# Kernel tuning notes

Measured on AMD Instinct MI355X. Metric: run time of the kernel, lower is better.

The kernel has to match this reference:

```python
import jax, jax.numpy as jnp
import numpy as np

E, B, D = 32, 8192, 256

def setup_inputs() -> dict:
    key = jax.random.key(0)
    k_x, k_c, k_s = jax.random.split(key, 3)
    x = jax.random.normal(k_x, (B, D), dtype=jnp.float32)
    # RandomUniform(-0.5, 0.5) init for both weights
    Centroids = jax.random.uniform(k_c, (E, 1, D), dtype=jnp.float32, minval=-0.5, maxval=0.5)
    A = jax.random.normal(k_s, (E, D, D), dtype=jnp.float32) * 0.1
    # well-conditioned (invertible) covariance-like matrices
    Sigmas = jnp.einsum('eij,ekj->eik', A, A) / D + jnp.eye(D, dtype=jnp.float32)[None]
    return {"x": x, "Centroids": Centroids, "Sigmas": Sigmas}

def reference(x, Centroids, Sigmas):
    # dif: [E, B, D] = broadcasted (x - centroid_e)
    dif = x[None, :, :] - Centroids            # Centroids [E,1,D] broadcasts over B
    inv = jnp.linalg.inv(Sigmas)               # [E, D, D]
    # diagonal of dif @ inv @ dif^T computed directly: [E, B]
    mah = jnp.einsum('ebd,edk,ebk->eb', dif, inv, dif)
    return mah.T                                # [B, E]; activation is None (linear)
```

## Files before the change

kernel.cpp:

```cpp
#include <hip/hip_runtime.h>
#include <stdint.h>


#define NE 32
#define NB 8192
#define DD 256

typedef __bf16 bf16_t;
typedef bf16_t bf16x8 __attribute__((ext_vector_type(8)));
typedef bf16_t bf16x4 __attribute__((ext_vector_type(4)));
typedef float  f32x4  __attribute__((ext_vector_type(4)));
typedef float  f32x16 __attribute__((ext_vector_type(16)));

#define LDX 264
#define LDT 264

static __device__ __forceinline__ void gl2lds16(const void* g, void* l) {
  __builtin_amdgcn_global_load_lds((__attribute__((address_space(1))) void*)(g),
                                   (__attribute__((address_space(3))) void*)(l),
                                   16, 0, 0);
}

__global__ __launch_bounds__(256) void k_x(const float* __restrict__ x,
                                           bf16_t* __restrict__ Xbf) {
  int i8 = (blockIdx.x * 256 + threadIdx.x) * 8;
  f32x4 a = *(const f32x4*)(x + i8);
  f32x4 b = *(const f32x4*)(x + i8 + 4);
  bf16x8 o;
  o[0] = (bf16_t)a[0]; o[1] = (bf16_t)a[1]; o[2] = (bf16_t)a[2]; o[3] = (bf16_t)a[3];
  o[4] = (bf16_t)b[0]; o[5] = (bf16_t)b[1]; o[6] = (bf16_t)b[2]; o[7] = (bf16_t)b[3];
  *(bf16x8*)(Xbf + i8) = o;
}

__global__ __launch_bounds__(512, 2) void k_inv(const float* __restrict__ Sg,
                                                bf16_t* __restrict__ Invbf) {
  int ct = blockIdx.x;
  int e  = blockIdx.y;
  int tid = threadIdx.x, w = tid >> 6, l = tid & 63;
  __shared__ bf16_t Ml[256 * LDX];
  __shared__ bf16_t T2t[32 * LDT];
  const float* Se = Sg + (size_t)e * 65536;

#pragma unroll
  for (int i = 0; i < 16; ++i) {
    int s = i * 512 + tid;
    int row = s >> 5, c8 = (s & 31) * 8;
    f32x4 a = *(const f32x4*)(Se + row * 256 + c8);
    f32x4 b = *(const f32x4*)(Se + row * 256 + c8 + 4);
    float v[8] = {a[0], a[1], a[2], a[3], b[0], b[1], b[2], b[3]};
    int dj = row - c8;
    if (dj >= 0 && dj < 8) v[dj] -= 1.0f;
    bf16x8 o;
#pragma unroll
    for (int j = 0; j < 8; ++j) o[j] = (bf16_t)v[j];
    *(bf16x8*)&Ml[row * LDX + c8] = o;
  }
  __syncthreads();

  int rA = w * 32 + (l & 15);
  int q8 = (l >> 4) * 8;
  int cg0 = ct * 32;

  f32x4 acc1[2][2];
#pragma unroll
  for (int i = 0; i < 2; ++i)
#pragma unroll
    for (int j = 0; j < 2; ++j) acc1[i][j] = (f32x4){0.f, 0.f, 0.f, 0.f};
#pragma unroll
  for (int kk = 0; kk < 256; kk += 32) {
    bf16x8 a0 = *(const bf16x8*)&Ml[rA * LDX + kk + q8];
    bf16x8 a1 = *(const bf16x8*)&Ml[(rA + 16) * LDX + kk + q8];
    bf16x8 b0 = *(const bf16x8*)&Ml[(cg0 + (l & 15)) * LDX + kk + q8];
    bf16x8 b1 = *(const bf16x8*)&Ml[(cg0 + 16 + (l & 15)) * LDX + kk + q8];
    acc1[0][0] = __builtin_amdgcn_mfma_f32_16x16x32_bf16(a0, b0, acc1[0][0], 0, 0, 0);
    acc1[0][1] = __builtin_amdgcn_mfma_f32_16x16x32_bf16(a0, b1, acc1[0][1], 0, 0, 0);
    acc1[1][0] = __builtin_amdgcn_mfma_f32_16x16x32_bf16(a1, b0, acc1[1][0], 0, 0, 0);
    acc1[1][1] = __builtin_amdgcn_mfma_f32_16x16x32_bf16(a1, b1, acc1[1][1], 0, 0, 0);
  }
#pragma unroll
  for (int nf = 0; nf < 2; ++nf) {
    int n0 = w * 32 + nf * 16 + (l >> 4) * 4;
#pragma unroll
    for (int cf = 0; cf < 2; ++cf) {
      int cl = cf * 16 + (l & 15), cg = cg0 + cl;
      bf16x4 mr = *(const bf16x4*)&Ml[cg * LDX + n0];
      f32x4 vv = acc1[nf][cf];
      bf16x4 o;
#pragma unroll
      for (int q = 0; q < 4; ++q) {
        float t2 = (((n0 + q) == cg) ? 1.0f : 0.0f) - (float)mr[q] + vv[q];
        o[q] = (bf16_t)t2;
      }
      *(bf16x4*)&T2t[cl * LDT + n0] = o;
    }
  }
  __syncthreads();

  f32x4 acc2[2][2];
#pragma unroll
  for (int i = 0; i < 2; ++i)
#pragma unroll
    for (int j = 0; j < 2; ++j) acc2[i][j] = (f32x4){0.f, 0.f, 0.f, 0.f};
#pragma unroll
  for (int kk = 0; kk < 256; kk += 32) {
    bf16x8 a0 = *(const bf16x8*)&Ml[rA * LDX + kk + q8];
    bf16x8 a1 = *(const bf16x8*)&Ml[(rA + 16) * LDX + kk + q8];
    bf16x8 b0 = *(const bf16x8*)&T2t[(l & 15) * LDT + kk + q8];
    bf16x8 b1 = *(const bf16x8*)&T2t[(16 + (l & 15)) * LDT + kk + q8];
    acc2[0][0] = __builtin_amdgcn_mfma_f32_16x16x32_bf16(a0, b0, acc2[0][0], 0, 0, 0);
    acc2[0][1] = __builtin_amdgcn_mfma_f32_16x16x32_bf16(a0, b1, acc2[0][1], 0, 0, 0);
    acc2[1][0] = __builtin_amdgcn_mfma_f32_16x16x32_bf16(a1, b0, acc2[1][0], 0, 0, 0);
    acc2[1][1] = __builtin_amdgcn_mfma_f32_16x16x32_bf16(a1, b1, acc2[1][1], 0, 0, 0);
  }
  bf16_t* Ce = Invbf + (size_t)e * 65536;
#pragma unroll
  for (int nf = 0; nf < 2; ++nf) {
    int n0 = w * 32 + nf * 16 + (l >> 4) * 4;
#pragma unroll
    for (int cf = 0; cf < 2; ++cf) {
      int cg = cg0 + cf * 16 + (l & 15);
#pragma unroll
      for (int q = 0; q < 4; ++q) {
        float vv = (((n0 + q) == cg) ? 1.0f : 0.0f) - acc2[nf][cf][q];
        Ce[(cg >> 3) * 2048 + (n0 + q) * 8 + (cg & 7)] = (bf16_t)vv;
      }
    }
  }
}

__global__ __launch_bounds__(256) void k_v(const bf16_t* __restrict__ Invbf,
                                           const float* __restrict__ Cent,
                                           float* __restrict__ v2,
                                           float* __restrict__ s_out) {
  int e = blockIdx.x, d = threadIdx.x;
  __shared__ float cl[256];
  __shared__ float ps[256];
  cl[d] = Cent[e * 256 + d];
  __syncthreads();
  const bf16_t* Ie = Invbf + (size_t)e * 65536 + d * 8;
  float acc = 0.f;
#pragma unroll
  for (int ksl = 0; ksl < 32; ++ksl) {
    bf16x8 r = *(const bf16x8*)(Ie + ksl * 2048);
#pragma unroll
    for (int j = 0; j < 8; ++j) acc += (float)r[j] * cl[ksl * 8 + j];
  }
  v2[e * 256 + d] = 2.0f * acc;
  ps[d] = cl[d] * acc;
  __syncthreads();
  for (int off = 128; off > 0; off >>= 1) {
    if (d < off) ps[d] += ps[d + off];
    __syncthreads();
  }
  if (d == 0) s_out[e] = ps[0];
}

__global__ __launch_bounds__(512, 2) void k_main(const bf16_t* __restrict__ Xbf,
                                                 const bf16_t* __restrict__ Invbf,
                                                 const float* __restrict__ v2g,
                                                 const float* __restrict__ sg,
                                                 float* __restrict__ out) {
  int bt = blockIdx.x;
  int eg = blockIdx.y;
  int tid = threadIdx.x, w = tid >> 6, l = tid & 63;
  __shared__ bf16_t Xl[65536];
  __shared__ bf16_t Invl[2][8192];

  const bf16_t* Xg = Xbf + (size_t)bt * 65536;
  char* Xb = (char*)Xl;

#pragma unroll
  for (int p = 0; p < 16; p += 4) {
    f32x4 t0[4];
#pragma unroll
    for (int i = 0; i < 4; ++i) {
      int s = (p + i) * 512 + tid;
      int row = s >> 5, c16 = s & 31;
      t0[i] = *(const f32x4*)(Xg + row * 256 + c16 * 8);
    }
#pragma unroll
    for (int i = 0; i < 4; ++i) {
      int s = (p + i) * 512 + tid;
      int row = s >> 5, c16 = s & 31;
      int byte = (row * 512 + c16 * 16) ^ ((row & 7) << 4);
      *(f32x4*)(Xb + byte) = t0[i];
    }
  }

  {
    const bf16_t* src = Invbf + (size_t)(eg * 4) * 65536;
    bf16_t* dst = (bf16_t*)Invl[0];
    gl2lds16(src + w * 512 + l * 8,        dst + w * 512);
    gl2lds16(src + 4096 + w * 512 + l * 8, dst + 4096 + w * 512);
  }
  __syncthreads();

  int wn = w >> 2, wb = w & 3;
  int lrow = l & 31, lhalf = l >> 5;
  int nbase = wn * 128;
  int bbase = wb * 64;

  f32x16 acc[4][2];
#pragma unroll
  for (int nf = 0; nf < 4; ++nf)
#pragma unroll
    for (int cf = 0; cf < 2; ++cf)
#pragma unroll
      for (int q = 0; q < 16; ++q) acc[nf][cf][q] = 0.f;

  for (int t = 0; t < 32; ++t) {
    int kk = (t & 7) * 32;
    int cur = t & 1;
    if (t < 31) {
      int tn = t + 1;
      const bf16_t* src = Invbf + (size_t)(eg * 4 + (tn >> 3)) * 65536 + (tn & 7) * 8192;
      bf16_t* dst = (bf16_t*)Invl[tn & 1];
      gl2lds16(src + w * 512 + l * 8,        dst + w * 512);
      gl2lds16(src + 4096 + w * 512 + l * 8, dst + 4096 + w * 512);
    }
    const bf16_t* Ib = (const bf16_t*)Invl[cur];
    bf16x8 af[2][4], bfr[2][2];
#pragma unroll
    for (int s = 0; s < 2; ++s) {
#pragma unroll
      for (int nf = 0; nf < 4; ++nf)
        af[s][nf] = *(const bf16x8*)(Ib + (s * 2 + lhalf) * 2048 + (nbase + nf * 32 + lrow) * 8);
#pragma unroll
      for (int cf = 0; cf < 2; ++cf) {
        int b = bbase + cf * 32 + lrow;
        int byte = (b * 512 + (kk + s * 16 + lhalf * 8) * 2) ^ ((b & 7) << 4);
        bfr[s][cf] = *(const bf16x8*)(Xb + byte);
      }
    }
#pragma unroll
    for (int s = 0; s < 2; ++s)
#pragma unroll
      for (int nf = 0; nf < 4; ++nf)
#pragma unroll
        for (int cf = 0; cf < 2; ++cf)
          acc[nf][cf] = __builtin_amdgcn_mfma_f32_32x32x16_bf16(af[s][nf], bfr[s][cf], acc[nf][cf], 0, 0, 0);

    if ((t & 7) == 7) {
      int e = eg * 4 + (t >> 3);
      float bsum[2] = {0.f, 0.f};
#pragma unroll
      for (int nf = 0; nf < 4; ++nf)
#pragma unroll
        for (int g = 0; g < 4; ++g) {
          int n0 = nbase + nf * 32 + 8 * g + 4 * lhalf;
          f32x4 vv = *(const f32x4*)(v2g + e * 256 + n0);
#pragma unroll
          for (int cf = 0; cf < 2; ++cf) {
            int b = bbase + cf * 32 + lrow;
            int byte = (b * 512 + n0 * 2) ^ ((b & 7) << 4);
            bf16x4 xr = *(const bf16x4*)(Xb + byte);
#pragma unroll
            for (int q = 0; q < 4; ++q)
              bsum[cf] += (float)xr[q] * (acc[nf][cf][g * 4 + q] - vv[q]);
          }
        }
      __syncthreads();
      float* red = (float*)Invl[cur];
#pragma unroll
      for (int cf = 0; cf < 2; ++cf) {
        float r = bsum[cf];
        r += __shfl_xor(r, 32);
        if (lhalf == 0) red[wn * 256 + bbase + cf * 32 + lrow] = r;
      }
      __syncthreads();
      if (tid < 256) {
        float res = sg[e] + red[tid] + red[256 + tid];
        out[(size_t)(bt * 256 + tid) * 32 + e] = res;
      }
#pragma unroll
      for (int nf = 0; nf < 4; ++nf)
#pragma unroll
        for (int cf = 0; cf < 2; ++cf)
#pragma unroll
          for (int q = 0; q < 16; ++q) acc[nf][cf][q] = 0.f;
    }
    __syncthreads();
  }
}

extern "C" void kernel_launch(void* const* d_in, const int* in_sizes, int n_in,
                              void* d_out, int out_size, void* d_ws, size_t ws_size,
                              hipStream_t stream) {
  const float* x    = (const float*)d_in[0];
  const float* cent = (const float*)d_in[1];
  const float* sig  = (const float*)d_in[2];
  float* out = (float*)d_out;

  char* ws = (char*)d_ws;
  bf16_t* Xbf   = (bf16_t*)(ws);
  bf16_t* Invbf = (bf16_t*)(ws + (4ull << 20));
  float*  v2    = (float*)(ws + (8ull << 20));
  float*  sArr  = (float*)(ws + (8ull << 20) + 32768);

  k_x   <<<dim3(1024),   dim3(256), 0, stream>>>(x, Xbf);
  k_inv <<<dim3(8, NE),  dim3(512), 0, stream>>>(sig, Invbf);
  k_v   <<<dim3(NE),     dim3(256), 0, stream>>>(Invbf, cent, v2, sArr);
  k_main<<<dim3(32, 8),  dim3(512), 0, stream>>>(Xbf, Invbf, v2, sArr, out);
}
```

Measured before the change: 72.37 us.

## Fold bf16 conversion of x into inversion kernel and shrink main tiles

Removes the separate x-to-bf16 kernel and does that conversion at the start of each inversion block, saving one launch. The main kernel now uses 128-row batch tiles with 256 threads, giving a 512-block grid instead of 256 blocks so more CUs stay busy. X is staged into LDS with direct global-to-LDS loads using a wider XOR swizzle, and the inverse is streamed in smaller 16-wide K chunks. In exchange there are more pipeline iterations and barriers per block, and each inverse tile is reloaded by twice as many blocks.

Measured after the change: 77.84 us. 1.08x slower.

```diff
diff --git a/kernel.cpp b/kernel.cpp
--- a/kernel.cpp
+++ b/kernel.cpp
@@ -21,18 +21,9 @@
                                    16, 0, 0);
 }
 
-__global__ __launch_bounds__(256) void k_x(const float* __restrict__ x,
-                                           bf16_t* __restrict__ Xbf) {
-  int i8 = (blockIdx.x * 256 + threadIdx.x) * 8;
-  f32x4 a = *(const f32x4*)(x + i8);
-  f32x4 b = *(const f32x4*)(x + i8 + 4);
-  bf16x8 o;
-  o[0] = (bf16_t)a[0]; o[1] = (bf16_t)a[1]; o[2] = (bf16_t)a[2]; o[3] = (bf16_t)a[3];
-  o[4] = (bf16_t)b[0]; o[5] = (bf16_t)b[1]; o[6] = (bf16_t)b[2]; o[7] = (bf16_t)b[3];
-  *(bf16x8*)(Xbf + i8) = o;
-}
-
 __global__ __launch_bounds__(512, 2) void k_inv(const float* __restrict__ Sg,
+                                                const float* __restrict__ x,
+                                                bf16_t* __restrict__ Xbf,
                                                 bf16_t* __restrict__ Invbf) {
   int ct = blockIdx.x;
   int e  = blockIdx.y;
@@ -40,6 +31,22 @@
   __shared__ bf16_t Ml[256 * LDX];
   __shared__ bf16_t T2t[32 * LDT];
   const float* Se = Sg + (size_t)e * 65536;
+
+  {
+    int off = (blockIdx.x + 8 * blockIdx.y) * 8192 + tid * 16;
+    f32x4 a0 = *(const f32x4*)(x + off);
+    f32x4 a1 = *(const f32x4*)(x + off + 4);
+    f32x4 a2 = *(const f32x4*)(x + off + 8);
+    f32x4 a3 = *(const f32x4*)(x + off + 12);
+    bf16x8 o0, o1;
+#pragma unroll
+    for (int j = 0; j < 4; ++j) {
+      o0[j] = (bf16_t)a0[j]; o0[4 + j] = (bf16_t)a1[j];
+      o1[j] = (bf16_t)a2[j]; o1[4 + j] = (bf16_t)a3[j];
+    }
+    *(bf16x8*)(Xbf + off) = o0;
+    *(bf16x8*)(Xbf + off + 8) = o1;
+  }
 
 #pragma unroll
   for (int i = 0; i < 16; ++i) {
@@ -155,47 +162,37 @@
   if (d == 0) s_out[e] = ps[0];
 }
 
-__global__ __launch_bounds__(512, 2) void k_main(const bf16_t* __restrict__ Xbf,
+__global__ __launch_bounds__(256, 2) void k_main(const bf16_t* __restrict__ Xbf,
                                                  const bf16_t* __restrict__ Invbf,
                                                  const float* __restrict__ v2g,
                                                  const float* __restrict__ sg,
                                                  float* __restrict__ out) {
-  int bt = blockIdx.x;
-  int eg = blockIdx.y;
+  int eg = blockIdx.x;
+  int bt = blockIdx.y;
   int tid = threadIdx.x, w = tid >> 6, l = tid & 63;
-  __shared__ bf16_t Xl[65536];
-  __shared__ bf16_t Invl[2][8192];
-
-  const bf16_t* Xg = Xbf + (size_t)bt * 65536;
+  __shared__ bf16_t Xl[128 * 256];
+  __shared__ bf16_t Invl[2][4096];
+
+  const bf16_t* Xg = Xbf + (size_t)bt * 128 * 256;
   char* Xb = (char*)Xl;
 
 #pragma unroll
-  for (int p = 0; p < 16; p += 4) {
-    f32x4 t0[4];
-#pragma unroll
-    for (int i = 0; i < 4; ++i) {
-      int s = (p + i) * 512 + tid;
-      int row = s >> 5, c16 = s & 31;
-      t0[i] = *(const f32x4*)(Xg + row * 256 + c16 * 8);
-    }
-#pragma unroll
-    for (int i = 0; i < 4; ++i) {
-      int s = (p + i) * 512 + tid;
-      int row = s >> 5, c16 = s & 31;
-      int byte = (row * 512 + c16 * 16) ^ ((row & 7) << 4);
-      *(f32x4*)(Xb + byte) = t0[i];
-    }
-  }
-
+  for (int j = 0; j < 16; ++j) {
+    int base = (w * 16 + j) * 1024;
+    int row = (base >> 9) + (l >> 5);
+    int inner = (l & 31) * 16;
+    const char* src = (const char*)Xg + row * 512 + (inner ^ ((row & 31) << 4));
+    gl2lds16(src, Xb + base);
+  }
   {
     const bf16_t* src = Invbf + (size_t)(eg * 4) * 65536;
     bf16_t* dst = (bf16_t*)Invl[0];
-    gl2lds16(src + w * 512 + l * 8,        dst + w * 512);
-    gl2lds16(src + 4096 + w * 512 + l * 8, dst + 4096 + w * 512);
-  }
-  __syncthreads();
-
-  int wn = w >> 2, wb = w & 3;
+    gl2lds16(src + w * 1024 + l * 8,       dst + w * 1024);
+    gl2lds16(src + w * 1024 + 512 + l * 8, dst + w * 1024 + 512);
+  }
+  __syncthreads();
+
+  int wn = w >> 1, wb = w & 1;
   int lrow = l & 31, lhalf = l >> 5;
   int nbase = wn * 128;
   int bbase = wb * 64;
@@ -208,40 +205,34 @@
 #pragma unroll
       for (int q = 0; q < 16; ++q) acc[nf][cf][q] = 0.f;
 
-  for (int t = 0; t < 32; ++t) {
-    int kk = (t & 7) * 32;
-    int cur = t & 1;
-    if (t < 31) {
-      int tn = t + 1;
-      const bf16_t* src = Invbf + (size_t)(eg * 4 + (tn >> 3)) * 65536 + (tn & 7) * 8192;
-      bf16_t* dst = (bf16_t*)Invl[tn & 1];
-      gl2lds16(src + w * 512 + l * 8,        dst + w * 512);
-      gl2lds16(src + 4096 + w * 512 + l * 8, dst + 4096 + w * 512);
-    }
-    const bf16_t* Ib = (const bf16_t*)Invl[cur];
-    bf16x8 af[2][4], bfr[2][2];
-#pragma unroll
-    for (int s = 0; s < 2; ++s) {
-#pragma unroll
-      for (int nf = 0; nf < 4; ++nf)
-        af[s][nf] = *(const bf16x8*)(Ib + (s * 2 + lhalf) * 2048 + (nbase + nf * 32 + lrow) * 8);
-#pragma unroll
-      for (int cf = 0; cf < 2; ++cf) {
-        int b = bbase + cf * 32 + lrow;
-        int byte = (b * 512 + (kk + s * 16 + lhalf * 8) * 2) ^ ((b & 7) << 4);
-        bfr[s][cf] = *(const bf16x8*)(Xb + byte);
-      }
-    }
-#pragma unroll
-    for (int s = 0; s < 2; ++s)
-#pragma unroll
-      for (int nf = 0; nf < 4; ++nf)
-#pragma unroll
-        for (int cf = 0; cf < 2; ++cf)
-          acc[nf][cf] = __builtin_amdgcn_mfma_f32_32x32x16_bf16(af[s][nf], bfr[s][cf], acc[nf][cf], 0, 0, 0);
-
-    if ((t & 7) == 7) {
-      int e = eg * 4 + (t >> 3);
+  for (int T = 0; T < 64; ++T) {
+    int c = T & 15, buf = T & 1;
+    if (T < 63) {
+      int Tn = T + 1;
+      const bf16_t* src = Invbf + (size_t)(eg * 4 + (Tn >> 4)) * 65536 + (Tn & 15) * 4096;
+      bf16_t* dst = (bf16_t*)Invl[Tn & 1];
+      gl2lds16(src + w * 1024 + l * 8,       dst + w * 1024);
+      gl2lds16(src + w * 1024 + 512 + l * 8, dst + w * 1024 + 512);
+    }
+    const bf16_t* Ib = (const bf16_t*)Invl[buf];
+    bf16x8 af[4], bfr[2];
+#pragma unroll
+    for (int nf = 0; nf < 4; ++nf)
+      af[nf] = *(const bf16x8*)(Ib + lhalf * 2048 + (nbase + nf * 32 + lrow) * 8);
+#pragma unroll
+    for (int cf = 0; cf < 2; ++cf) {
+      int b = bbase + cf * 32 + lrow;
+      int byte = (b * 512 + c * 32 + lhalf * 16) ^ ((b & 31) << 4);
+      bfr[cf] = *(const bf16x8*)(Xb + byte);
+    }
+#pragma unroll
+    for (int nf = 0; nf < 4; ++nf)
+#pragma unroll
+      for (int cf = 0; cf < 2; ++cf)
+        acc[nf][cf] = __builtin_amdgcn_mfma_f32_32x32x16_bf16(af[nf], bfr[cf], acc[nf][cf], 0, 0, 0);
+
+    if (c == 15) {
+      int e = eg * 4 + (T >> 4);
       float bsum[2] = {0.f, 0.f};
 #pragma unroll
       for (int nf = 0; nf < 4; ++nf)
@@ -252,7 +243,7 @@
 #pragma unroll
           for (int cf = 0; cf < 2; ++cf) {
             int b = bbase + cf * 32 + lrow;
-            int byte = (b * 512 + n0 * 2) ^ ((b & 7) << 4);
+            int byte = (b * 512 + n0 * 2) ^ ((b & 31) << 4);
             bf16x4 xr = *(const bf16x4*)(Xb + byte);
 #pragma unroll
             for (int q = 0; q < 4; ++q)
@@ -260,17 +251,17 @@
           }
         }
       __syncthreads();
-      float* red = (float*)Invl[cur];
+      float* red = (float*)Invl[buf];
 #pragma unroll
       for (int cf = 0; cf < 2; ++cf) {
         float r = bsum[cf];
         r += __shfl_xor(r, 32);
-        if (lhalf == 0) red[wn * 256 + bbase + cf * 32 + lrow] = r;
+        if (lhalf == 0) red[wn * 128 + bbase + cf * 32 + lrow] = r;
       }
       __syncthreads();
-      if (tid < 256) {
-        float res = sg[e] + red[tid] + red[256 + tid];
-        out[(size_t)(bt * 256 + tid) * 32 + e] = res;
+      if (tid < 128) {
+        float res = sg[e] + red[tid] + red[128 + tid];
+        out[(size_t)(bt * 128 + tid) * 32 + e] = res;
       }
 #pragma unroll
       for (int nf = 0; nf < 4; ++nf)
@@ -297,8 +288,7 @@
   float*  v2    = (float*)(ws + (8ull << 20));
   float*  sArr  = (float*)(ws + (8ull << 20) + 32768);
 
-  k_x   <<<dim3(1024),   dim3(256), 0, stream>>>(x, Xbf);
-  k_inv <<<dim3(8, NE),  dim3(512), 0, stream>>>(sig, Invbf);
+  k_inv <<<dim3(8, NE),  dim3(512), 0, stream>>>(sig, x, Xbf, Invbf);
   k_v   <<<dim3(NE),     dim3(256), 0, stream>>>(Invbf, cent, v2, sArr);
-  k_main<<<dim3(32, 8),  dim3(512), 0, stream>>>(Xbf, Invbf, v2, sArr, out);
-}
+  k_main<<<dim3(8, 64),  dim3(256), 0, stream>>>(Xbf, Invbf, v2, sArr, out);
+}
```
